# Kernel tuning notes

Measured on AMD Instinct MI355X. Metric: run time of the kernel, lower is better.

The kernel has to match this reference:

```python
import jax, jax.numpy as jnp
import numpy as np
import math

NUM_HEADS = 8
DIM_Q = 512
DIM_K = 512
DIM_V = 512
EPS = 1e-5


def _layernorm(x, g, b):
    mu = jnp.mean(x, axis=-1, keepdims=True)
    var = jnp.mean(jnp.square(x - mu), axis=-1, keepdims=True)
    return (x - mu) * jax.lax.rsqrt(var + EPS) * g + b


def setup_inputs() -> dict:
    key = jax.random.key(0)
    ks = jax.random.split(key, 16)
    B, Nq, Nk = 8, 1024, 1024
    s_q = 1.0 / math.sqrt(DIM_Q)
    s_v = 1.0 / math.sqrt(DIM_V)
    return {
        "Q": jax.random.normal(ks[0], (B, Nq, DIM_Q), jnp.float32),
        "K": jax.random.normal(ks[1], (B, Nk, DIM_K), jnp.float32),
        "Wq": jax.random.uniform(ks[2], (DIM_Q, DIM_V), jnp.float32, -s_q, s_q),
        "bq": jax.random.uniform(ks[3], (DIM_V,), jnp.float32, -s_q, s_q),
        "Wk": jax.random.uniform(ks[4], (DIM_K, DIM_V), jnp.float32, -s_q, s_q),
        "bk": jax.random.uniform(ks[5], (DIM_V,), jnp.float32, -s_q, s_q),
        "Wv": jax.random.uniform(ks[6], (DIM_K, DIM_V), jnp.float32, -s_q, s_q),
        "bv": jax.random.uniform(ks[7], (DIM_V,), jnp.float32, -s_q, s_q),
        "Wo": jax.random.uniform(ks[8], (DIM_V, DIM_V), jnp.float32, -s_v, s_v),
        "bo": jax.random.uniform(ks[9], (DIM_V,), jnp.float32, -s_v, s_v),
        "g0": jnp.ones((DIM_V,), jnp.float32),
        "b0": jnp.zeros((DIM_V,), jnp.float32),
        "g1": jnp.ones((DIM_V,), jnp.float32),
        "b1": jnp.zeros((DIM_V,), jnp.float32),
        "M": jax.random.randint(ks[10], (B, Nq, Nk), 0, 2, jnp.int32),
    }


def reference(Q, K, Wq, bq, Wk, bk, Wv, bv, Wo, bo, g0, b0, g1, b1, M):
    B, Nq, _ = Q.shape
    Nk = K.shape[1]
    H = NUM_HEADS
    d = DIM_V // H
    # projections
    Qp = Q @ Wq + bq                      # [B,Nq,Dv]
    Kp = K @ Wk + bk                      # [B,Nk,Dv]
    Vp = K @ Wv + bv                      # [B,Nk,Dv]
    # split heads: channel h*d+j -> head h (matches torch split/cat ordering)
    Qh = Qp.reshape(B, Nq, H, d)
    Kh = Kp.reshape(B, Nk, H, d)
    Vh = Vp.reshape(B, Nk, H, d)
    # scores scaled by sqrt(dim_V) (faithful to original, NOT sqrt(head_dim))
    A = jnp.einsum("bqhd,bkhd->bhqk", Qh, Kh) / math.sqrt(DIM_V)
    A = jnp.where(M[:, None, :, :] == 0, -jnp.inf, A)
    A = jax.nn.softmax(A, axis=-1)
    # residual add of the (projected, per-head) query, then merge heads
    O = Qh + jnp.einsum("bhqk,bkhd->bqhd", A, Vh)
    O = O.reshape(B, Nq, DIM_V)
    O = _layernorm(O, g0, b0)
    O = O + jax.nn.relu(O @ Wo + bo)
    O = _layernorm(O, g1, b1)
    return O
```

## Files before the change

kernel.cpp:

```cpp
#include <hip/hip_runtime.h>

typedef unsigned short u16;
typedef unsigned int u32;
typedef unsigned long long u64;
typedef __attribute__((ext_vector_type(8))) short short8;
typedef __attribute__((ext_vector_type(4))) float f32x4;
typedef __attribute__((ext_vector_type(4))) u32 u32x4;

#define BATCH 8
#define NSEQ 1024
#define DMODEL 512
#define HDIM 64
#define SCALE_LOG2E 0.06375871114929199f
#define FIXED_MAX 16.0f

#define O_QBF 0ULL
#define O_KBF 8388608ULL
#define O_WB  16777216ULL
#define O_QP  19922944ULL
#define O_KP  28311552ULL
#define O_VP  36700160ULL

__device__ __forceinline__ u16 f2bf(float f) {
  u32 u = __float_as_uint(f);
  u = (u + 0x7fffu + ((u >> 16) & 1u)) >> 16;
  return (u16)u;
}
__device__ __forceinline__ float bf2f(u16 s) {
  return __uint_as_float(((u32)s) << 16);
}
__device__ __forceinline__ void gload16(const void* g, void* l) {
  __builtin_amdgcn_global_load_lds((const __attribute__((address_space(1))) void*)g,
                                   (__attribute__((address_space(3))) void*)l, 16, 0, 0);
}
__device__ __forceinline__ u32 cvtpk(float a, float b) {
  u32 r;
  asm("v_cvt_pk_bf16_f32 %0, %1, %2" : "=v"(r) : "v"(a), "v"(b));
  return r;
}

__global__ __launch_bounds__(256) void prep_kernel(
    const float* __restrict__ Q, const float* __restrict__ K,
    const float* __restrict__ Wq, const float* __restrict__ Wk,
    const float* __restrict__ Wv, const float* __restrict__ Wo,
    const int* __restrict__ M,
    u16* __restrict__ Qbf, u16* __restrict__ Kbf, u16* __restrict__ Wb,
    u16* __restrict__ Mbias)
{
  __shared__ float lds[64 * 68];
  const int bi = blockIdx.x, t = threadIdx.x;
  if (bi < 4096) {
    const float* src = (bi < 2048) ? Q : K;
    u16* dst = (bi < 2048) ? Qbf : Kbf;
    const int lb = bi & 2047;
    const size_t base = ((size_t)lb * 256 + t) * 8;
    float4 a = *(const float4*)(src + base);
    float4 c = *(const float4*)(src + base + 4);
    short8 o;
    o[0] = (short)f2bf(a.x); o[1] = (short)f2bf(a.y);
    o[2] = (short)f2bf(a.z); o[3] = (short)f2bf(a.w);
    o[4] = (short)f2bf(c.x); o[5] = (short)f2bf(c.y);
    o[6] = (short)f2bf(c.z); o[7] = (short)f2bf(c.w);
    *(short8*)(dst + base) = o;
  } else if (bi < 4352) {
    const int qid = bi - 4096;
    const int w = qid >> 6;
    const int tt = qid & 63;
    const int tr = tt >> 3, tc = tt & 7;
    const float* W = (w == 0) ? Wq : (w == 1) ? Wk : (w == 2) ? Wv : Wo;
#pragma unroll
    for (int j = 0; j < 4; ++j) {
      int vi = j * 256 + t;
      int row = vi >> 4, c4 = vi & 15;
      float4 v = *(const float4*)(W + (size_t)(tr * 64 + row) * 512 + tc * 64 + c4 * 4);
      lds[row * 68 + c4 * 4 + 0] = v.x;
      lds[row * 68 + c4 * 4 + 1] = v.y;
      lds[row * 68 + c4 * 4 + 2] = v.z;
      lds[row * 68 + c4 * 4 + 3] = v.w;
    }
    __syncthreads();
#pragma unroll
    for (int j = 0; j < 2; ++j) {
      int oi = j * 256 + t;
      int nl = oi >> 3, k8 = oi & 7;
      short8 o;
#pragma unroll
      for (int i = 0; i < 8; ++i) o[i] = (short)f2bf(lds[(k8 * 8 + i) * 68 + nl]);
      *(short8*)(Wb + (size_t)w * 262144 + (size_t)(tc * 64 + nl) * 512 + tr * 64 + k8 * 8) = o;
    }
  } else {
    const int pb = bi - 4352;
    const size_t idx = ((size_t)pb * 256 + t) * 16;
    const int4* Ms = (const int4*)(M + idx);
    int4 m0 = Ms[0], m1 = Ms[1], m2 = Ms[2], m3 = Ms[3];
    int mv[16] = {m0.x, m0.y, m0.z, m0.w, m1.x, m1.y, m1.z, m1.w,
                  m2.x, m2.y, m2.z, m2.w, m3.x, m3.y, m3.z, m3.w};
    short8 o0, o1;
#pragma unroll
    for (int i = 0; i < 8; ++i) {
      o0[i] = mv[i] ? (short)0 : (short)0xC700;
      o1[i] = mv[8 + i] ? (short)0 : (short)0xC700;
    }
    *(short8*)(Mbias + idx) = o0;
    *(short8*)(Mbias + idx + 8) = o1;
  }
}

template<int MODE>
__global__ __launch_bounds__(256) void gemm_bt(
    const u16* __restrict__ Aq, const u16* __restrict__ Ak,
    const u16* __restrict__ Wb,
    const float* __restrict__ b0, const float* __restrict__ b1, const float* __restrict__ b2,
    u16* __restrict__ outp, const u16* __restrict__ resid)
{
  __shared__ __align__(16) char Alds[8192];
  __shared__ __align__(16) char Blds[8192];
  const int tid = threadIdx.x;
  const int wv = tid >> 6, lane = tid & 63;
  const int g16 = lane >> 4, l16 = lane & 15;
  const int wr = wv >> 1, wc = wv & 1;
  const int bx = blockIdx.x, by = blockIdx.y, bz = blockIdx.z;

  const u16* A; const u16* W; const float* bias; u16* out;
  if (MODE == 0) {
    A = (bz == 0) ? Aq : Ak;
    W = Wb + (size_t)bz * 262144;
    bias = (bz == 0) ? b0 : ((bz == 1) ? b1 : b2);
    out = outp + (size_t)bz * 4194304;
  } else {
    A = Aq; W = Wb; bias = b0; out = outp;
  }

  const int m0 = bx * 128, n0 = by * 128;
  f32x4 acc[4][4] = {};

  for (int kt = 0; kt < 16; ++kt) {
    const int k0 = kt * 32;
#pragma unroll
    for (int r = 0; r < 2; ++r) {
      int idx = r * 256 + tid;
      int row = idx >> 2, sl = idx & 3;
      gload16(A + (size_t)(m0 + row) * 512 + k0 + sl * 8, Alds + r * 4096 + wv * 1024);
      gload16(W + (size_t)(n0 + row) * 512 + k0 + sl * 8, Blds + r * 4096 + wv * 1024);
    }
    __syncthreads();
    short8 af[4], bfr[4];
#pragma unroll
    for (int mt = 0; mt < 4; ++mt)
      af[mt] = *(const short8*)(Alds + (wr * 64 + mt * 16 + l16) * 64 + g16 * 16);
#pragma unroll
    for (int nt = 0; nt < 4; ++nt)
      bfr[nt] = *(const short8*)(Blds + (wc * 64 + nt * 16 + l16) * 64 + g16 * 16);
#pragma unroll
    for (int mt = 0; mt < 4; ++mt)
#pragma unroll
      for (int nt = 0; nt < 4; ++nt)
        acc[mt][nt] = __builtin_amdgcn_mfma_f32_16x16x32_bf16(af[mt], bfr[nt], acc[mt][nt], 0, 0, 0);
    __syncthreads();
  }

#pragma unroll
  for (int nt = 0; nt < 4; ++nt) {
    int col = n0 + wc * 64 + nt * 16 + l16;
    float bcol = bias[col];
#pragma unroll
    for (int mt = 0; mt < 4; ++mt) {
#pragma unroll
      for (int r = 0; r < 4; ++r) {
        int row = m0 + wr * 64 + mt * 16 + g16 * 4 + r;
        float v = acc[mt][nt][r] + bcol;
        if (MODE == 1) {
          v = fmaxf(v, 0.f) + bf2f(resid[(size_t)row * 512 + col]);
        }
        out[(size_t)row * 512 + col] = f2bf(v);
      }
    }
  }
}

__global__ __launch_bounds__(256, 2) void attn_kernel(
    const u16* __restrict__ Qp, const u16* __restrict__ Kp, const u16* __restrict__ Vp,
    const u16* __restrict__ Mbias, u16* __restrict__ O1)
{
  __shared__ __align__(16) char K_lds[2][8192];
  __shared__ __align__(16) char VT_lds[2][8192];
  __shared__ __align__(16) char PT_lds[4][2][2048];

  const int tid = threadIdx.x;
  const int wv = tid >> 6, lane = tid & 63;
  const int g16 = lane >> 4, l16 = lane & 15;
  const int l7 = l16 & 7;

  const int wg = blockIdx.x;
  const int swz = (wg & 7) * 64 + (wg >> 3);
  const int qt = swz & 7;
  const int h = (swz >> 3) & 7;
  const int b = swz >> 6;
  const int qg = qt * 128;
  const int hb = h * HDIM;
  const size_t batch_row = (size_t)b * NSEQ;

  const int qbase = qg + wv * 32;
  const int dv2 = (tid & 31) * 2;
  const int kg = tid >> 5;

  short8 b_q[2][2];
#pragma unroll
  for (int m = 0; m < 2; ++m)
#pragma unroll
    for (int c = 0; c < 2; ++c) {
      short8 raw = *(const short8*)(Qp + (batch_row + qbase + m * 16 + l16) * DMODEL +
                                    hb + c * 32 + g16 * 8);
      short8 sc;
#pragma unroll
      for (int j = 0; j < 8; ++j) sc[j] = (short)f2bf(bf2f((u16)raw[j]) * SCALE_LOG2E);
      b_q[m][c] = sc;
    }

  const u64* Mq0 = (const u64*)(Mbias + (batch_row + qbase + l16) * 1024);
  const u64* Mq1 = (const u64*)(Mbias + (batch_row + qbase + 16 + l16) * 1024);

  auto stageK = [&](int kt2, char* dst) {
#pragma unroll
    for (int r = 0; r < 2; ++r) {
      int idx = r * 256 + tid;
      int row = idx >> 3, sl = idx & 7;
      int chunk = sl ^ (row & 7);
      gload16(Kp + (batch_row + kt2 * 64 + row) * DMODEL + hb + chunk * 8,
              dst + r * 4096 + wv * 1024);
    }
  };
  auto loadV = [&](int kt2, u32* vr) {
#pragma unroll
    for (int j = 0; j < 8; ++j)
      vr[j] = *(const u32*)(Vp + (batch_row + kt2 * 64 + kg * 8 + j) * DMODEL + hb + dv2);
  };
  auto writeVT = [&](const u32* vr, char* dstv) {
    u32x4 lo, hi;
#pragma unroll
    for (int i = 0; i < 4; ++i) {
      lo[i] = __builtin_amdgcn_perm(vr[2 * i + 1], vr[2 * i], 0x05040100u);
      hi[i] = __builtin_amdgcn_perm(vr[2 * i + 1], vr[2 * i], 0x07060302u);
    }
    *(u32x4*)(dstv + dv2 * 128 + ((kg ^ (dv2 & 7)) << 4)) = lo;
    *(u32x4*)(dstv + (dv2 + 1) * 128 + ((kg ^ ((dv2 + 1) & 7)) << 4)) = hi;
  };
  auto loadBias = [&](int kt2, u64* bb) {
#pragma unroll
    for (int kf = 0; kf < 4; ++kf) {
      bb[kf] = Mq0[kt2 * 16 + kf * 4 + g16];
      bb[4 + kf] = Mq1[kt2 * 16 + kf * 4 + g16];
    }
  };

  float lL[2] = {0.f, 0.f};
  f32x4 accO[2][4] = {};
  char* Pw0 = &PT_lds[wv][0][0];
  char* Pw1 = &PT_lds[wv][1][0];

  u32 vreg[8];
  u64 bias_cur[8], bias_next[8];
  stageK(0, &K_lds[0][0]);
  loadV(0, vreg);
  loadBias(0, bias_cur);
  writeVT(vreg, &VT_lds[0][0]);
  loadV(1, vreg);

  for (int kt = 0; kt < 16; ++kt) {
    __syncthreads();
    char* Kc = &K_lds[kt & 1][0];
    char* Vc = &VT_lds[kt & 1][0];
    if (kt < 15) {
      writeVT(vreg, &VT_lds[(kt + 1) & 1][0]);
      stageK(kt + 1, &K_lds[(kt + 1) & 1][0]);
      loadBias(kt + 1, bias_next);
    }
    if (kt < 14) loadV(kt + 2, vreg);

    f32x4 s_[2][4];
    __builtin_amdgcn_s_setprio(1);
#pragma unroll
    for (int kf = 0; kf < 4; ++kf) {
      int row = kf * 16 + l16;
      short8 ak0 = *(const short8*)(Kc + row * 128 + ((g16 ^ l7) << 4));
      short8 ak1 = *(const short8*)(Kc + row * 128 + (((4 + g16) ^ l7) << 4));
#pragma unroll
      for (int m = 0; m < 2; ++m) {
        u64 bv = bias_cur[m * 4 + kf];
        u32 blo = (u32)bv, bhi = (u32)(bv >> 32);
        f32x4 acc;
        acc[0] = __uint_as_float(blo << 16);
        acc[1] = __uint_as_float(blo & 0xffff0000u);
        acc[2] = __uint_as_float(bhi << 16);
        acc[3] = __uint_as_float(bhi & 0xffff0000u);
        acc = __builtin_amdgcn_mfma_f32_16x16x32_bf16(ak0, b_q[m][0], acc, 0, 0, 0);
        acc = __builtin_amdgcn_mfma_f32_16x16x32_bf16(ak1, b_q[m][1], acc, 0, 0, 0);
        s_[m][kf] = acc;
      }
    }
    __builtin_amdgcn_s_setprio(0);

#pragma unroll
    for (int m = 0; m < 2; ++m) {
      char* Pw = (m == 0) ? Pw0 : Pw1;
      float sum = 0.f;
#pragma unroll
      for (int kf = 0; kf < 4; ++kf) {
        float e0 = __builtin_amdgcn_exp2f(s_[m][kf][0] - FIXED_MAX);
        float e1 = __builtin_amdgcn_exp2f(s_[m][kf][1] - FIXED_MAX);
        float e2 = __builtin_amdgcn_exp2f(s_[m][kf][2] - FIXED_MAX);
        float e3 = __builtin_amdgcn_exp2f(s_[m][kf][3] - FIXED_MAX);
        sum += (e0 + e1) + (e2 + e3);
        int chunk = kf * 2 + (g16 >> 1);
        int off = l16 * 128 + ((chunk ^ l7) << 4) + (g16 & 1) * 8;
        u32 c0 = cvtpk(e0, e1);
        u32 c1 = cvtpk(e2, e3);
        *(u64*)(Pw + off) = (u64)c0 | ((u64)c1 << 32);
      }
      lL[m] += sum;
    }

    short8 b_p[2][2];
#pragma unroll
    for (int kc = 0; kc < 2; ++kc) {
      b_p[0][kc] = *(const short8*)(Pw0 + l16 * 128 + (((kc * 4 + g16) ^ l7) << 4));
      b_p[1][kc] = *(const short8*)(Pw1 + l16 * 128 + (((kc * 4 + g16) ^ l7) << 4));
    }
    __builtin_amdgcn_s_setprio(1);
#pragma unroll
    for (int f = 0; f < 4; ++f) {
      int vrow = f * 16 + l16;
      short8 av0 = *(const short8*)(Vc + vrow * 128 + ((g16 ^ l7) << 4));
      short8 av1 = *(const short8*)(Vc + vrow * 128 + (((4 + g16) ^ l7) << 4));
#pragma unroll
      for (int m = 0; m < 2; ++m) {
        accO[m][f] = __builtin_amdgcn_mfma_f32_16x16x32_bf16(av0, b_p[m][0], accO[m][f], 0, 0, 0);
        accO[m][f] = __builtin_amdgcn_mfma_f32_16x16x32_bf16(av1, b_p[m][1], accO[m][f], 0, 0, 0);
      }
    }
    __builtin_amdgcn_s_setprio(0);

    if (kt < 15) {
#pragma unroll
      for (int i = 0; i < 8; ++i) bias_cur[i] = bias_next[i];
    }
  }

#pragma unroll
  for (int m = 0; m < 2; ++m) {
    float l = lL[m];
    l += __shfl_xor(l, 16, 64);
    l += __shfl_xor(l, 32, 64);
    float inv = 1.0f / fmaxf(l, 1e-20f);
    int q = qbase + m * 16 + l16;
#pragma unroll
    for (int f = 0; f < 4; ++f) {
      size_t o = (batch_row + q) * DMODEL + hb + f * 16 + g16 * 4;
      u64 qh = *(const u64*)(Qp + o);
      u64 ov = 0;
#pragma unroll
      for (int r = 0; r < 4; ++r) {
        float val = accO[m][f][r] * inv + bf2f((u16)(qh >> (r * 16)));
        ov |= ((u64)f2bf(val)) << (r * 16);
      }
      *(u64*)(O1 + o) = ov;
    }
  }
}

template<int OUTF>
__global__ __launch_bounds__(256) void ln_kernel(
    const u16* __restrict__ X, const float* __restrict__ g, const float* __restrict__ bb,
    void* __restrict__ outv)
{
  const int tid = threadIdx.x;
  const int wv = tid >> 6, lane = tid & 63;
  const size_t row = (size_t)blockIdx.x * 4 + wv;
  short8 x8 = *(const short8*)(X + row * 512 + lane * 8);
  float xf[8];
  float s = 0.f, s2 = 0.f;
#pragma unroll
  for (int i = 0; i < 8; ++i) {
    xf[i] = bf2f((u16)x8[i]);
    s += xf[i];
    s2 += xf[i] * xf[i];
  }
#pragma unroll
  for (int d = 1; d < 64; d <<= 1) {
    s += __shfl_xor(s, d, 64);
    s2 += __shfl_xor(s2, d, 64);
  }
  float mu = s * (1.f / 512.f);
  float var = s2 * (1.f / 512.f) - mu * mu;
  float rs = rsqrtf(var + 1e-5f);
  float4 ga = *(const float4*)(g + lane * 8);
  float4 gb = *(const float4*)(g + lane * 8 + 4);
  float4 ba = *(const float4*)(bb + lane * 8);
  float4 bc = *(const float4*)(bb + lane * 8 + 4);
  float gv[8] = {ga.x, ga.y, ga.z, ga.w, gb.x, gb.y, gb.z, gb.w};
  float bv[8] = {ba.x, ba.y, ba.z, ba.w, bc.x, bc.y, bc.z, bc.w};
  float y[8];
#pragma unroll
  for (int i = 0; i < 8; ++i) y[i] = (xf[i] - mu) * rs * gv[i] + bv[i];
  if (OUTF) {
    float* o = (float*)outv + row * 512 + lane * 8;
    float4 o1 = {y[0], y[1], y[2], y[3]};
    float4 o2 = {y[4], y[5], y[6], y[7]};
    *(float4*)o = o1;
    *(float4*)(o + 4) = o2;
  } else {
    short8 o;
#pragma unroll
    for (int i = 0; i < 8; ++i) o[i] = (short)f2bf(y[i]);
    *(short8*)((u16*)outv + row * 512 + lane * 8) = o;
  }
}

extern "C" void kernel_launch(void* const* d_in, const int* in_sizes, int n_in,
                              void* d_out, int out_size, void* d_ws, size_t ws_size,
                              hipStream_t stream) {
  (void)in_sizes; (void)n_in; (void)out_size; (void)ws_size;
  const float* Q  = (const float*)d_in[0];
  const float* K  = (const float*)d_in[1];
  const float* Wq = (const float*)d_in[2];
  const float* bq = (const float*)d_in[3];
  const float* Wk = (const float*)d_in[4];
  const float* bk = (const float*)d_in[5];
  const float* Wv = (const float*)d_in[6];
  const float* bv = (const float*)d_in[7];
  const float* Wo = (const float*)d_in[8];
  const float* bo = (const float*)d_in[9];
  const float* g0 = (const float*)d_in[10];
  const float* b0 = (const float*)d_in[11];
  const float* g1 = (const float*)d_in[12];
  const float* b1 = (const float*)d_in[13];
  const int*   M  = (const int*)d_in[14];
  float* out = (float*)d_out;
  char* ws = (char*)d_ws;

  u16* Qbf = (u16*)(ws + O_QBF);
  u16* Kbf = (u16*)(ws + O_KBF);
  u16* Wb  = (u16*)(ws + O_WB);
  u16* Qp  = (u16*)(ws + O_QP);
  u16* Kp  = (u16*)(ws + O_KP);
  u16* Vp  = (u16*)(ws + O_VP);
  u16* Mbias = (u16*)d_out;
  u16* O1  = Kbf;
  u16* Xn  = Qp;
  u16* Z   = Qbf;

  prep_kernel<<<6400, 256, 0, stream>>>(Q, K, Wq, Wk, Wv, Wo, M, Qbf, Kbf, Wb, Mbias);
  gemm_bt<0><<<dim3(64, 4, 3), 256, 0, stream>>>(Qbf, Kbf, Wb, bq, bk, bv, Qp, nullptr);
  attn_kernel<<<512, 256, 0, stream>>>(Qp, Kp, Vp, Mbias, O1);
  ln_kernel<0><<<2048, 256, 0, stream>>>(O1, g0, b0, (void*)Xn);
  gemm_bt<1><<<dim3(64, 4, 1), 256, 0, stream>>>(Xn, nullptr, Wb + 3 * 262144, bo,
                                                 nullptr, nullptr, Z, Xn);
  ln_kernel<1><<<2048, 256, 0, stream>>>(Z, g1, b1, (void*)out);
}
```

Baseline: 113.1 us.

## Ping-pong register buffers and explicit partial waitcnt in attention K-loop

Restructures the attention key-tile loop into an unrolled pair of tile calls that alternate between two register buffers for V and mask-bias prefetches. This removes the per-iteration bias copy and lets the next V load be issued into a separate buffer. The implicit __syncthreads is replaced by an explicit s_waitcnt vmcnt(8) plus s_barrier so that outstanding global loads for later tiles need not drain at each barrier. The risk is that the hand-set vmcnt count may not match the actual number of in-flight loads, which would break correctness or force extra stalls, and full unrolling raises code size and register pressure.

After: 188.7 us. +66.9%, slower.

```diff
diff --git a/kernel.cpp b/kernel.cpp
--- a/kernel.cpp
+++ b/kernel.cpp
@@ -230,12 +230,12 @@
               dst + r * 4096 + wv * 1024);
     }
   };
-  auto loadV = [&](int kt2, u32* vr) {
+  auto loadV = [&](int kt2, u32 (&vr)[8]) {
 #pragma unroll
     for (int j = 0; j < 8; ++j)
       vr[j] = *(const u32*)(Vp + (batch_row + kt2 * 64 + kg * 8 + j) * DMODEL + hb + dv2);
   };
-  auto writeVT = [&](const u32* vr, char* dstv) {
+  auto writeVT = [&](const u32 (&vr)[8], char* dstv) {
     u32x4 lo, hi;
 #pragma unroll
     for (int i = 0; i < 4; ++i) {
@@ -245,7 +245,7 @@
     *(u32x4*)(dstv + dv2 * 128 + ((kg ^ (dv2 & 7)) << 4)) = lo;
     *(u32x4*)(dstv + (dv2 + 1) * 128 + ((kg ^ ((dv2 + 1) & 7)) << 4)) = hi;
   };
-  auto loadBias = [&](int kt2, u64* bb) {
+  auto loadBias = [&](int kt2, u64 (&bb)[8]) {
 #pragma unroll
     for (int kf = 0; kf < 4; ++kf) {
       bb[kf] = Mq0[kt2 * 16 + kf * 4 + g16];
@@ -258,24 +258,29 @@
   char* Pw0 = &PT_lds[wv][0][0];
   char* Pw1 = &PT_lds[wv][1][0];
 
-  u32 vreg[8];
-  u64 bias_cur[8], bias_next[8];
+  u32 vregA[8], vregB[8];
+  u64 biasA[8], biasB[8];
+
   stageK(0, &K_lds[0][0]);
-  loadV(0, vreg);
-  loadBias(0, bias_cur);
-  writeVT(vreg, &VT_lds[0][0]);
-  loadV(1, vreg);
-
-  for (int kt = 0; kt < 16; ++kt) {
-    __syncthreads();
-    char* Kc = &K_lds[kt & 1][0];
-    char* Vc = &VT_lds[kt & 1][0];
+  loadV(0, vregA);
+  loadBias(0, biasA);
+  writeVT(vregA, &VT_lds[0][0]);
+  loadV(1, vregA);
+
+  auto tile = [&](int kt, int CUR, u32 (&vin)[8], u32 (&vout)[8], u64 (&bin)[8],
+                  u64 (&bout)[8]) {
+    asm volatile("s_waitcnt vmcnt(8) lgkmcnt(0)" ::: "memory");
+    __builtin_amdgcn_sched_barrier(0);
+    __builtin_amdgcn_s_barrier();
+    __builtin_amdgcn_sched_barrier(0);
+    char* Kc = &K_lds[CUR][0];
+    char* Vc = &VT_lds[CUR][0];
     if (kt < 15) {
-      writeVT(vreg, &VT_lds[(kt + 1) & 1][0]);
-      stageK(kt + 1, &K_lds[(kt + 1) & 1][0]);
-      loadBias(kt + 1, bias_next);
-    }
-    if (kt < 14) loadV(kt + 2, vreg);
+      writeVT(vin, &VT_lds[CUR ^ 1][0]);
+      stageK(kt + 1, &K_lds[CUR ^ 1][0]);
+      loadV(kt + 2 < 16 ? kt + 2 : 15, vout);
+      loadBias(kt + 1, bout);
+    }
 
     f32x4 s_[2][4];
     __builtin_amdgcn_s_setprio(1);
@@ -286,7 +291,7 @@
       short8 ak1 = *(const short8*)(Kc + row * 128 + (((4 + g16) ^ l7) << 4));
 #pragma unroll
       for (int m = 0; m < 2; ++m) {
-        u64 bv = bias_cur[m * 4 + kf];
+        u64 bv = bin[m * 4 + kf];
         u32 blo = (u32)bv, bhi = (u32)(bv >> 32);
         f32x4 acc;
         acc[0] = __uint_as_float(blo << 16);
@@ -339,11 +344,12 @@
       }
     }
     __builtin_amdgcn_s_setprio(0);
-
-    if (kt < 15) {
-#pragma unroll
-      for (int i = 0; i < 8; ++i) bias_cur[i] = bias_next[i];
-    }
+  };
+
+#pragma unroll
+  for (int t = 0; t < 8; ++t) {
+    tile(2 * t, 0, vregA, vregB, biasA, biasB);
+    tile(2 * t + 1, 1, vregB, vregA, biasB, biasA);
   }
 
 #pragma unroll
```
